# Optimization experiments

Hardware: AMD Instinct MI355X
Metric: run time of the kernel (lower is better)

The kernel has to match this reference:

```python
import jax, jax.numpy as jnp
import numpy as np

# ---- module hyper-params (match init_kwargs) ----
B, C_IN, C_OUT, K, H, W = 16, 128, 128, 3, 56, 56
M, G, STRIDE, RED = 2, 2, 1, 16
R = max(RED, C_IN // RED)            # GC_Attention bottleneck width = 16
MO = M * C_OUT                       # gc_att output channels
GROUPS = G * C_OUT                   # grouped 1x1 fc groups = 256
IN_PG = MO // GROUPS                 # in channels per group = M // G = 1
COUT_FC = C_OUT * C_IN * K * K       # generated weight elements per sample
OUT_PG = COUT_FC // GROUPS           # out channels per group = 576
PAD = K // 2
LN_EPS = 1e-5


def setup_inputs() -> dict:
    key = jax.random.key(0)
    ks = jax.random.split(key, 6)
    sc = 0.05
    return {
        "x": jax.random.normal(ks[0], (B, C_IN, H, W), jnp.float32),
        # GC_Attention: conv_mask (1x1, C->1)
        "w_mask": jax.random.normal(ks[1], (C_IN,), jnp.float32) * sc,
        "b_mask": jnp.zeros((), jnp.float32),
        # transform: conv1x1 C->R, LayerNorm(R), ReLU, conv1x1 R->M*out
        "w1": jax.random.normal(ks[2], (R, C_IN), jnp.float32) * sc,
        "b1": jnp.zeros((R,), jnp.float32),
        "ln_g": jnp.ones((R,), jnp.float32),
        "ln_b": jnp.zeros((R,), jnp.float32),
        "w2": jax.random.normal(ks[3], (MO, R), jnp.float32) * sc,
        "b2": jnp.zeros((MO,), jnp.float32),
        # fc: grouped 1x1 conv, groups=G*out, stored [groups, out_pg, in_pg]
        "w_fc": jax.random.normal(ks[4], (GROUPS, OUT_PG, IN_PG), jnp.float32) * sc,
        "b_fc": jnp.zeros((COUT_FC,), jnp.float32),
    }


def reference(x, w_mask, b_mask, w1, b1, ln_g, ln_b, w2, b2, w_fc, b_fc):
    b, c, h, w = x.shape
    # --- GC_Attention: global-context pooling via spatial softmax ---
    mask = jnp.einsum('bchw,c->bhw', x, w_mask) + b_mask        # [b,h,w]
    att = jax.nn.softmax(mask.reshape(b, -1), axis=-1)          # [b,hw]
    ctx = jnp.einsum('bcs,bs->bc', x.reshape(b, c, -1), att)    # [b,C]
    # bottleneck transform (1x1 convs on [b,*,1,1] == dense layers)
    t = ctx @ w1.T + b1                                          # [b,R]
    mu = t.mean(-1, keepdims=True)
    var = t.var(-1, keepdims=True)
    t = (t - mu) / jnp.sqrt(var + LN_EPS) * ln_g + ln_b          # LayerNorm over R
    t = jax.nn.relu(t)
    a = jax.nn.sigmoid(t @ w2.T + b2)                            # [b, M*out]
    # --- grouped 1x1 conv: generate per-sample conv weights ---
    xw = jnp.einsum('bgi,goi->bgo', a.reshape(b, GROUPS, IN_PG), w_fc)
    xw = xw.reshape(b, COUT_FC) + b_fc
    Wd = xw.reshape(b, C_OUT, C_IN, K, K)                        # per-sample kernels
    # --- per-sample conv2d (torch: groups=b on batch-folded input) ---
    def conv1(xi, wi):
        return jax.lax.conv_general_dilated(
            xi[None], wi, (STRIDE, STRIDE), [(PAD, PAD), (PAD, PAD)],
            dimension_numbers=('NCHW', 'OIHW', 'NCHW'))[0]
    return jax.vmap(conv1)(x, Wd)                                # [b, out, H, W]
```

## Files before the change

kernel.cpp:

```cpp
#include <hip/hip_runtime.h>
#include <hip/hip_bf16.h>
#include <math.h>

#define BATCH 16
#define CIN   128
#define COUT  128
#define SS    3136
#define XT_ROW 8192
#define XT_PER_B (58*XT_ROW)
#define NKB   18

typedef __attribute__((ext_vector_type(8))) __bf16 bf16x8;
typedef __attribute__((ext_vector_type(4))) float  floatx4;

static __device__ __forceinline__ unsigned short f2bf(float f) {
  union { float f; unsigned u; } v; v.f = f;
  unsigned r = v.u + 0x7fffu + ((v.u >> 16) & 1u);
  return (unsigned short)(r >> 16);
}
static __device__ __forceinline__ float bf2f(unsigned short u) {
  union { unsigned u; float f; } v; v.u = ((unsigned)u) << 16; return v.f;
}

static __device__ __forceinline__ float waveReduceSum(float v) {
  #pragma unroll
  for (int off = 32; off > 0; off >>= 1) v += __shfl_xor(v, off, 64);
  return v;
}

static __device__ __forceinline__ void load_lds16(const void* g, void* l) {
  __builtin_amdgcn_global_load_lds(
      (const __attribute__((address_space(1))) void*)g,
      (__attribute__((address_space(3))) void*)l, 16, 0, 0);
}

static __device__ __forceinline__ void barrier_fenced() {
  asm volatile("" ::: "memory");
  __builtin_amdgcn_s_barrier();
  asm volatile("" ::: "memory");
}

static __device__ __forceinline__ int sswz(int ci) {
  return (ci ^ (ci >> 4)) & 15;
}

__global__ __launch_bounds__(256, 4)
void k0_padT(const float* __restrict__ x, const float* __restrict__ w_mask,
             const float* __restrict__ b_mask,
             unsigned short* __restrict__ xT, float* __restrict__ rowsum,
             float* __restrict__ pctx) {
  int b = blockIdx.y, prow = blockIdx.x, t = threadIdx.x;
  int y = prow - 1;
  __shared__ __align__(16) unsigned short sx[128 * 64];
  __shared__ float swm[128];
  __shared__ float red[4 * 56];
  __shared__ float se[56];
  bool rowvalid = ((unsigned)y < 56u);

  if (!rowvalid) {
    unsigned short* dst = xT + (size_t)(b * 58 + prow) * XT_ROW;
    uint4 z4 = make_uint4(0u, 0u, 0u, 0u);
    #pragma unroll
    for (int q = 0; q < 4; q++)
      *reinterpret_cast<uint4*>(dst + (size_t)(t + 256 * q) * 8) = z4;
    if (t == 0) rowsum[b * 58 + prow] = 0.f;
    if (t < 128) pctx[(size_t)(b * 58 + prow) * 128 + t] = 0.f;
    return;
  }

  if (t < 128) swm[t] = w_mask[t];
  #pragma unroll
  for (int i = 0; i < 7; i++) {
    int c = t + 256 * i;
    int ci = c / 14, j = c - ci * 14;
    const float4 v = *reinterpret_cast<const float4*>(
        x + (size_t)(b * 128 + ci) * SS + y * 56 + j * 4);
    union { unsigned short s[4]; uint2 u; } pk;
    pk.s[0] = f2bf(v.x); pk.s[1] = f2bf(v.y);
    pk.s[2] = f2bf(v.z); pk.s[3] = f2bf(v.w);
    int blk = j ^ sswz(ci);
    *reinterpret_cast<uint2*>(&sx[ci * 64 + (blk << 2)]) = pk.u;
  }
  __syncthreads();

  if (t < 224) {
    int xx = t % 56, g = t / 56;
    float acc = 0.f;
    #pragma unroll
    for (int k = 0; k < 32; k++) {
      int ci = g * 32 + k;
      acc += bf2f(sx[ci * 64 + ((((xx >> 2) ^ sswz(ci)) << 2) | (xx & 3))]) * swm[ci];
    }
    red[g * 56 + xx] = acc;
  }
  __syncthreads();

  float e = 0.f;
  if (t < 56) {
    float m = red[t] + red[56 + t] + red[112 + t] + red[168 + t] + b_mask[0];
    e = expf(m);
    se[t] = e;
  }
  if (t < 64) {
    float s = waveReduceSum(e);
    if (t == 0) rowsum[b * 58 + prow] = s;
  }

  {
    int pcol = t >> 2, cig = t & 3;
    int xx = pcol - 1;
    bool colv = ((unsigned)xx < 56u);
    unsigned short tmp[32];
    #pragma unroll
    for (int i = 0; i < 32; i++) {
      int ci = cig * 32 + i;
      tmp[i] = colv ? sx[ci * 64 + ((((xx >> 2) ^ sswz(ci)) << 2) | (xx & 3))]
                    : (unsigned short)0;
    }
    unsigned short* dst = xT + ((size_t)(b * 58 + prow) * 64 + pcol) * 128 + cig * 32;
    #pragma unroll
    for (int q = 0; q < 4; q++)
      *reinterpret_cast<uint4*>(dst + q * 8) = *reinterpret_cast<const uint4*>(tmp + q * 8);
  }
  __syncthreads();

  {
    int c = t >> 1, h = t & 1;
    float acc = 0.f;
    #pragma unroll
    for (int j = 0; j < 28; j++) {
      int col = h * 28 + j;
      acc += bf2f(sx[c * 64 + ((((col >> 2) ^ sswz(c)) << 2) | (col & 3))]) * se[col];
    }
    acc += __shfl_xor(acc, 1, 64);
    if (h == 0) pctx[(size_t)(b * 58 + prow) * 128 + c] = acc;
  }
}

__global__ void k4_mlp(const float* __restrict__ rowsum, float* __restrict__ pctx,
                       const float* __restrict__ w1, const float* __restrict__ b1,
                       const float* __restrict__ ln_g, const float* __restrict__ ln_b,
                       const float* __restrict__ w2, const float* __restrict__ b2) {
  int b = blockIdx.x, t = threadIdx.x;
  __shared__ float sc[128], st[16], sn[16], shz;
  float rv = (t < 58) ? rowsum[b * 58 + t] : 0.f;
  float acc = 0.f;
  #pragma unroll
  for (int r = 0; r < 58; r++) acc += pctx[(size_t)(b * 58 + r) * 128 + t];
  if (t < 64) {
    float z = waveReduceSum(rv);
    if (t == 0) shz = 1.0f / z;
  }
  __syncthreads();
  sc[t] = acc * shz;
  __syncthreads();
  if (t < 16) {
    float s = b1[t];
    #pragma unroll 8
    for (int c = 0; c < 128; c++) s += sc[c] * w1[t * 128 + c];
    st[t] = s;
  }
  __syncthreads();
  if (t < 16) {
    float mu = 0.f, m2 = 0.f;
    #pragma unroll
    for (int r = 0; r < 16; r++) { float v = st[r]; mu += v; m2 += v * v; }
    mu *= (1.f / 16.f); m2 *= (1.f / 16.f);
    float rstd = rsqrtf(m2 - mu * mu + 1e-5f);
    float v = (st[t] - mu) * rstd * ln_g[t] + ln_b[t];
    sn[t] = fmaxf(v, 0.f);
  }
  __syncthreads();
  #pragma unroll
  for (int k = 0; k < 2; k++) {
    int mo = t + 128 * k;
    float s = b2[mo];
    #pragma unroll
    for (int r = 0; r < 16; r++) s += sn[r] * w2[mo * 16 + r];
    pctx[(size_t)b * (58 * 128) + mo] = 1.f / (1.f + expf(-s));
  }
}

__global__ void k5_wgen(const float* __restrict__ w_fc, const float* __restrict__ b_fc,
                        const float* __restrict__ abuf, unsigned short* __restrict__ wd) {
  int co = blockIdx.x, bp = blockIdx.y, t = threadIdx.x;
  int ci = t & 127, bb = t >> 7, b = bp * 2 + bb;
  __shared__ unsigned short sw[2][1152];
  const float* wr = w_fc + co * 1152 + ci * 9;
  const float* br = b_fc + co * 1152 + ci * 9;
  float a = abuf[(size_t)b * (58 * 128) + 2 * co + (ci >> 6)];
  int kq = ci & 63;
  int pos = (((kq >> 3) ^ (co & 7)) << 3) | (kq & 7);
  int kb0 = ci >> 6;
  #pragma unroll
  for (int khw = 0; khw < 9; khw++) {
    float v = a * wr[khw] + br[khw];
    sw[bb][(khw * 2 + kb0) * 64 + pos] = f2bf(v);
  }
  __syncthreads();
  for (int c = t; c < 288; c += 256) {
    int row = c / 144, q = c - row * 144;
    unsigned short* dst = wd + (size_t)((bp * 2 + row) * 128 + co) * 1152 + q * 8;
    *reinterpret_cast<uint4*>(dst) = *reinterpret_cast<const uint4*>(&sw[row][q * 8]);
  }
}

__global__ __launch_bounds__(512, 4) void k6_conv(const unsigned short* __restrict__ xT,
                                                  const unsigned short* __restrict__ wd,
                                                  float* __restrict__ out) {
  __shared__ __align__(16) unsigned short As[2][8192];
  __shared__ __align__(16) unsigned short Bs[2][8192];
  int t = threadIdx.x;
  int b = blockIdx.y, y0 = blockIdx.x * 2;
  int wave = t >> 6, lane = t & 63, l15 = lane & 15, quad = lane >> 4;
  int x7 = lane & 7;
  const unsigned short* wp  = wd + (size_t)b * (128 * 1152);
  const unsigned short* xTb = xT + (size_t)b * XT_PER_B;

  int ch0 = wave * 128 + lane, ch1 = ch0 + 64;
  int offA0 = (ch0 >> 3) * 1152 + (ch0 & 7) * 8;
  int offA1 = (ch1 >> 3) * 1152 + (ch1 & 7) * 8;
  int s0 = ch0 >> 3, s1 = ch1 >> 3;
  int c_ = lane & 7;
  int sr0 = s0 / 56, sc0 = s0 - sr0 * 56; if (sr0 >= 2) { sr0 = 0; sc0 = 0; }
  int sr1 = s1 / 56, sc1 = s1 - sr1 * 56; if (sr1 >= 2) { sr1 = 0; sc1 = 0; }
  int offB0 = (y0 + sr0) * XT_ROW + sc0 * 128 + (c_ ^ (s0 & 7)) * 8;
  int offB1 = (y0 + sr1) * XT_ROW + sc1 * 128 + (c_ ^ (s1 & 7)) * 8;

  int s_base = (wave & 3) * 32;
  int co_b   = (wave >> 2) * 64;

  floatx4 acc[4][2];
  floatx4 zero = {0.f, 0.f, 0.f, 0.f};
  #pragma unroll
  for (int i = 0; i < 4; i++)
    #pragma unroll
    for (int j = 0; j < 2; j++) acc[i][j] = zero;

  auto stage = [&](int buf, int kb) {
    int khw = kb >> 1;
    int kh = khw / 3;
    int kw = khw - kh * 3;
    int dB = kh * XT_ROW + kw * 128 + ((kb & 1) << 6);
    int dA = kb * 64;
    load_lds16(wp + offA0 + dA, &As[buf][wave * 1024]);
    load_lds16(wp + offA1 + dA, &As[buf][wave * 1024 + 512]);
    load_lds16(xTb + offB0 + dB, &Bs[buf][wave * 1024]);
    load_lds16(xTb + offB1 + dB, &Bs[buf][wave * 1024 + 512]);
  };

  stage(0, 0);
  for (int kb = 0; kb < NKB; kb++) {
    int cur = kb & 1;
    if (kb + 1 < NKB) {
      stage(cur ^ 1, kb + 1);
      asm volatile("s_waitcnt vmcnt(4)" ::: "memory");
    } else {
      asm volatile("s_waitcnt vmcnt(0)" ::: "memory");
    }
    barrier_fenced();
    __builtin_amdgcn_s_setprio(1);
    #pragma unroll
    for (int kk = 0; kk < 2; kk++) {
      bf16x8 af[4], bfr[2];
      int pc = ((kk * 4 + quad) ^ x7) << 3;
      #pragma unroll
      for (int i = 0; i < 4; i++)
        af[i] = *reinterpret_cast<const bf16x8*>(&As[cur][(co_b + i * 16 + l15) * 64 + pc]);
      #pragma unroll
      for (int j = 0; j < 2; j++)
        bfr[j] = *reinterpret_cast<const bf16x8*>(&Bs[cur][(s_base + j * 16 + l15) * 64 + pc]);
      #pragma unroll
      for (int i = 0; i < 4; i++)
        #pragma unroll
        for (int j = 0; j < 2; j++)
          acc[i][j] = __builtin_amdgcn_mfma_f32_16x16x32_bf16(af[i], bfr[j], acc[i][j], 0, 0, 0);
    }
    __builtin_amdgcn_s_setprio(0);
    barrier_fenced();
  }

  float* ob = out + (size_t)b * COUT * SS + y0 * 56;
  #pragma unroll
  for (int i = 0; i < 4; i++) {
    #pragma unroll
    for (int j = 0; j < 2; j++) {
      int sl = s_base + j * 16 + l15;
      if (sl < 112) {
        int row = (sl >= 56) ? 1 : 0;
        int col = sl - row * 56;
        #pragma unroll
        for (int r = 0; r < 4; r++) {
          int co = co_b + i * 16 + quad * 4 + r;
          ob[(size_t)co * SS + row * 56 + col] = acc[i][j][r];
        }
      }
    }
  }
}

extern "C" void kernel_launch(void* const* d_in, const int* in_sizes, int n_in,
                              void* d_out, int out_size, void* d_ws, size_t ws_size,
                              hipStream_t stream) {
  const float* x      = (const float*)d_in[0];
  const float* w_mask = (const float*)d_in[1];
  const float* b_mask = (const float*)d_in[2];
  const float* w1     = (const float*)d_in[3];
  const float* b1     = (const float*)d_in[4];
  const float* ln_g   = (const float*)d_in[5];
  const float* ln_b   = (const float*)d_in[6];
  const float* w2     = (const float*)d_in[7];
  const float* b2     = (const float*)d_in[8];
  const float* w_fc   = (const float*)d_in[9];
  const float* b_fc   = (const float*)d_in[10];
  float* out = (float*)d_out;

  char* ws = (char*)d_ws;
  unsigned short* xT  = (unsigned short*)(ws);
  unsigned short* wdw = (unsigned short*)(ws + 15204352);
  float* rowsum = (float*)(ws + 19922944);
  float* pctx   = (float*)(ws + 19927040);

  k0_padT<<<dim3(58, 16),  dim3(256), 0, stream>>>(x, w_mask, b_mask, xT, rowsum, pctx);
  k4_mlp <<<dim3(16),      dim3(128), 0, stream>>>(rowsum, pctx, w1, b1, ln_g, ln_b, w2, b2);
  k5_wgen<<<dim3(128, 8),  dim3(256), 0, stream>>>(w_fc, b_fc, pctx, wdw);
  k6_conv<<<dim3(28, 16),  dim3(512), 0, stream>>>(xT, wdw, out);
}
```

Before: 132.7 us.

## Fuse MLP into weight generation and remap conv blocks per XCD

The per-sample MLP (context normalisation, bottleneck, LayerNorm, sigmoid) is folded into the weight-generation kernel. Each block recomputes the MLP for its two samples and keeps only the two attention values it needs, which removes one kernel launch and the global round trip through pctx. This is paid for by redundant MLP work, about 128x per sample, including re-reading 58x128 partial context values in every block. Separately, the conv grid is flattened to one dimension and block ids are mapped so each XCD handles two whole batches, aiming for better L2 reuse of weights and input.

```diff
diff --git a/kernel.cpp b/kernel.cpp
--- a/kernel.cpp
+++ b/kernel.cpp
@@ -137,65 +137,65 @@
   }
 }
 
-__global__ void k4_mlp(const float* __restrict__ rowsum, float* __restrict__ pctx,
-                       const float* __restrict__ w1, const float* __restrict__ b1,
-                       const float* __restrict__ ln_g, const float* __restrict__ ln_b,
-                       const float* __restrict__ w2, const float* __restrict__ b2) {
-  int b = blockIdx.x, t = threadIdx.x;
-  __shared__ float sc[128], st[16], sn[16], shz;
-  float rv = (t < 58) ? rowsum[b * 58 + t] : 0.f;
+__global__ void k5m(const float* __restrict__ rowsum, const float* __restrict__ pctx,
+                    const float* __restrict__ w1, const float* __restrict__ b1,
+                    const float* __restrict__ ln_g, const float* __restrict__ ln_b,
+                    const float* __restrict__ w2, const float* __restrict__ b2,
+                    const float* __restrict__ w_fc, const float* __restrict__ b_fc,
+                    unsigned short* __restrict__ wd) {
+  int co = blockIdx.x, bp = blockIdx.y, t = threadIdx.x;
+  int bh = t >> 7, tt = t & 127;
+  int b = bp * 2 + bh;
+  __shared__ unsigned short sw[2][1152];
+  __shared__ float sc[2][128], st[2][16], sn[2][16], sa[2][2], shz[2];
+
   float acc = 0.f;
   #pragma unroll
-  for (int r = 0; r < 58; r++) acc += pctx[(size_t)(b * 58 + r) * 128 + t];
-  if (t < 64) {
-    float z = waveReduceSum(rv);
-    if (t == 0) shz = 1.0f / z;
-  }
-  __syncthreads();
-  sc[t] = acc * shz;
-  __syncthreads();
-  if (t < 16) {
-    float s = b1[t];
+  for (int r = 0; r < 58; r++) acc += pctx[(size_t)(b * 58 + r) * 128 + tt];
+  if ((t & 64) == 0) {
+    float rv = (tt < 58) ? rowsum[b * 58 + tt] : 0.f;
+    float s = waveReduceSum(rv);
+    if (tt == 0) shz[bh] = 1.0f / s;
+  }
+  __syncthreads();
+  sc[bh][tt] = acc * shz[bh];
+  __syncthreads();
+  if (tt < 16) {
+    float s = b1[tt];
     #pragma unroll 8
-    for (int c = 0; c < 128; c++) s += sc[c] * w1[t * 128 + c];
-    st[t] = s;
-  }
-  __syncthreads();
-  if (t < 16) {
+    for (int c = 0; c < 128; c++) s += sc[bh][c] * w1[tt * 128 + c];
+    st[bh][tt] = s;
+  }
+  __syncthreads();
+  if (tt < 16) {
     float mu = 0.f, m2 = 0.f;
     #pragma unroll
-    for (int r = 0; r < 16; r++) { float v = st[r]; mu += v; m2 += v * v; }
+    for (int r = 0; r < 16; r++) { float v = st[bh][r]; mu += v; m2 += v * v; }
     mu *= (1.f / 16.f); m2 *= (1.f / 16.f);
     float rstd = rsqrtf(m2 - mu * mu + 1e-5f);
-    float v = (st[t] - mu) * rstd * ln_g[t] + ln_b[t];
-    sn[t] = fmaxf(v, 0.f);
-  }
-  __syncthreads();
-  #pragma unroll
-  for (int k = 0; k < 2; k++) {
-    int mo = t + 128 * k;
+    float v = (st[bh][tt] - mu) * rstd * ln_g[tt] + ln_b[tt];
+    sn[bh][tt] = fmaxf(v, 0.f);
+  }
+  __syncthreads();
+  if (tt < 2) {
+    int mo = 2 * co + tt;
     float s = b2[mo];
     #pragma unroll
-    for (int r = 0; r < 16; r++) s += sn[r] * w2[mo * 16 + r];
-    pctx[(size_t)b * (58 * 128) + mo] = 1.f / (1.f + expf(-s));
-  }
-}
-
-__global__ void k5_wgen(const float* __restrict__ w_fc, const float* __restrict__ b_fc,
-                        const float* __restrict__ abuf, unsigned short* __restrict__ wd) {
-  int co = blockIdx.x, bp = blockIdx.y, t = threadIdx.x;
-  int ci = t & 127, bb = t >> 7, b = bp * 2 + bb;
-  __shared__ unsigned short sw[2][1152];
-  const float* wr = w_fc + co * 1152 + ci * 9;
-  const float* br = b_fc + co * 1152 + ci * 9;
-  float a = abuf[(size_t)b * (58 * 128) + 2 * co + (ci >> 6)];
-  int kq = ci & 63;
+    for (int r = 0; r < 16; r++) s += sn[bh][r] * w2[mo * 16 + r];
+    sa[bh][tt] = 1.f / (1.f + expf(-s));
+  }
+  __syncthreads();
+
+  const float* wr = w_fc + co * 1152 + tt * 9;
+  const float* br = b_fc + co * 1152 + tt * 9;
+  float a = sa[bh][tt >> 6];
+  int kq = tt & 63;
   int pos = (((kq >> 3) ^ (co & 7)) << 3) | (kq & 7);
-  int kb0 = ci >> 6;
+  int kb0 = tt >> 6;
   #pragma unroll
   for (int khw = 0; khw < 9; khw++) {
     float v = a * wr[khw] + br[khw];
-    sw[bb][(khw * 2 + kb0) * 64 + pos] = f2bf(v);
+    sw[bh][(khw * 2 + kb0) * 64 + pos] = f2bf(v);
   }
   __syncthreads();
   for (int c = t; c < 288; c += 256) {
@@ -211,7 +211,10 @@
   __shared__ __align__(16) unsigned short As[2][8192];
   __shared__ __align__(16) unsigned short Bs[2][8192];
   int t = threadIdx.x;
-  int b = blockIdx.y, y0 = blockIdx.x * 2;
+  int id = blockIdx.x;
+  int xcd = id & 7, j = id >> 3;
+  int b  = 2 * xcd + (j >= 28 ? 1 : 0);
+  int y0 = (j >= 28 ? j - 28 : j) * 2;
   int wave = t >> 6, lane = t & 63, l15 = lane & 15, quad = lane >> 4;
   int x7 = lane & 7;
   const unsigned short* wp  = wd + (size_t)b * (128 * 1152);
@@ -235,7 +238,7 @@
   #pragma unroll
   for (int i = 0; i < 4; i++)
     #pragma unroll
-    for (int j = 0; j < 2; j++) acc[i][j] = zero;
+    for (int j2 = 0; j2 < 2; j2++) acc[i][j2] = zero;
 
   auto stage = [&](int buf, int kb) {
     int khw = kb >> 1;
@@ -268,13 +271,13 @@
       for (int i = 0; i < 4; i++)
         af[i] = *reinterpret_cast<const bf16x8*>(&As[cur][(co_b + i * 16 + l15) * 64 + pc]);
       #pragma unroll
-      for (int j = 0; j < 2; j++)
-        bfr[j] = *reinterpret_cast<const bf16x8*>(&Bs[cur][(s_base + j * 16 + l15) * 64 + pc]);
+      for (int j2 = 0; j2 < 2; j2++)
+        bfr[j2] = *reinterpret_cast<const bf16x8*>(&Bs[cur][(s_base + j2 * 16 + l15) * 64 + pc]);
       #pragma unroll
       for (int i = 0; i < 4; i++)
         #pragma unroll
-        for (int j = 0; j < 2; j++)
-          acc[i][j] = __builtin_amdgcn_mfma_f32_16x16x32_bf16(af[i], bfr[j], acc[i][j], 0, 0, 0);
+        for (int j2 = 0; j2 < 2; j2++)
+          acc[i][j2] = __builtin_amdgcn_mfma_f32_16x16x32_bf16(af[i], bfr[j2], acc[i][j2], 0, 0, 0);
     }
     __builtin_amdgcn_s_setprio(0);
     barrier_fenced();
@@ -284,15 +287,15 @@
   #pragma unroll
   for (int i = 0; i < 4; i++) {
     #pragma unroll
-    for (int j = 0; j < 2; j++) {
-      int sl = s_base + j * 16 + l15;
+    for (int j2 = 0; j2 < 2; j2++) {
+      int sl = s_base + j2 * 16 + l15;
       if (sl < 112) {
         int row = (sl >= 56) ? 1 : 0;
         int col = sl - row * 56;
         #pragma unroll
         for (int r = 0; r < 4; r++) {
           int co = co_b + i * 16 + quad * 4 + r;
-          ob[(size_t)co * SS + row * 56 + col] = acc[i][j][r];
+          ob[(size_t)co * SS + row * 56 + col] = acc[i][j2][r];
         }
       }
     }
@@ -322,7 +325,7 @@
   float* pctx   = (float*)(ws + 19927040);
 
   k0_padT<<<dim3(58, 16),  dim3(256), 0, stream>>>(x, w_mask, b_mask, xT, rowsum, pctx);
-  k4_mlp <<<dim3(16),      dim3(128), 0, stream>>>(rowsum, pctx, w1, b1, ln_g, ln_b, w2, b2);
-  k5_wgen<<<dim3(128, 8),  dim3(256), 0, stream>>>(w_fc, b_fc, pctx, wdw);
-  k6_conv<<<dim3(28, 16),  dim3(512), 0, stream>>>(xT, wdw, out);
-}
+  k5m    <<<dim3(128, 8),  dim3(256), 0, stream>>>(rowsum, pctx, w1, b1, ln_g, ln_b,
+                                                   w2, b2, w_fc, b_fc, wdw);
+  k6_conv<<<dim3(448),     dim3(512), 0, stream>>>(xT, wdw, out);
+}
```

Result: no change. 133.8 us (+0.8%).
